# Optimization experiments

Measured on AMD Instinct MI355X. Metric: run time of the kernel, lower is better.

## Reference

```python
import jax, jax.numpy as jnp
import numpy as np

B, T, N, F_IN, C = 4, 40, 5000, 90, 256
E = 160000


def setup_inputs() -> dict:
    key = jax.random.key(0)
    ks = jax.random.split(key, 16)
    def p(k, shape, s=0.05):
        return jax.random.normal(k, shape, dtype=jnp.float32) * s
    z = lambda n: jnp.zeros((n,), jnp.float32)
    return {
        "x": jax.random.normal(ks[0], (B, T, N, F_IN), dtype=jnp.float32),
        "edge_index": jax.random.randint(ks[1], (1, 2, E), 0, N),
        "follower_ids": jax.random.randint(ks[2], (B,), 0, N),
        "attention": p(ks[3], (T,), 1.0),
        "Wz": p(ks[4], (F_IN, C)), "bz": z(C),
        "Wr": p(ks[5], (F_IN, C)), "br": z(C),
        "Wh": p(ks[6], (F_IN, C)), "bh": z(C),
        "Lz_w": p(ks[7], (2 * C, C)), "Lz_b": z(C),
        "Lr_w": p(ks[8], (2 * C, C)), "Lr_b": z(C),
        "Lh_w": p(ks[9], (2 * C, C)), "Lh_b": z(C),
        "M1_w": p(ks[10], (C, 64)), "M1_b": z(64),
        "M2_w": p(ks[11], (64, 32)), "M2_b": z(32),
        "M3_w": p(ks[12], (32, 5)), "M3_b": z(5),
    }


def _gcn_norm(edge_index, num_nodes):
    # GCNConv default: add self loops (weight 1), symmetric D^-1/2 (A+I) D^-1/2
    row, col = edge_index[0], edge_index[1]
    loop = jnp.arange(num_nodes)
    row = jnp.concatenate([row, loop])
    col = jnp.concatenate([col, loop])
    w = jnp.ones(row.shape[0], jnp.float32)
    deg = jnp.zeros(num_nodes, jnp.float32).at[col].add(w)
    dis = jnp.where(deg > 0, deg ** -0.5, 0.0)
    norm = dis[row] * w * dis[col]
    return row, col, norm


def _gcn(x, W, b, row, col, norm):
    # x: [B, N, F]; linear first, then normalized scatter-add aggregation
    xw = x @ W                                  # [B, N, C]
    msg = xw[:, row, :] * norm[None, :, None]   # [B, E+N, C]
    out = jnp.zeros_like(xw).at[:, col, :].add(msg)
    return out + b


def reference(x, edge_index, follower_ids, attention,
              Wz, bz, Wr, br, Wh, bh,
              Lz_w, Lz_b, Lr_w, Lr_b, Lh_w, Lh_b,
              M1_w, M1_b, M2_w, M2_b, M3_w, M3_b):
    ei = edge_index[0]
    row, col, norm = _gcn_norm(ei, N)

    def cell(H, xt):
        Z = jax.nn.sigmoid(jnp.concatenate([_gcn(xt, Wz, bz, row, col, norm), H], -1) @ Lz_w + Lz_b)
        R = jax.nn.sigmoid(jnp.concatenate([_gcn(xt, Wr, br, row, col, norm), H], -1) @ Lr_w + Lr_b)
        Ht = jnp.tanh(jnp.concatenate([_gcn(xt, Wh, bh, row, col, norm), H * R], -1) @ Lh_w + Lh_b)
        return Z * H + (1.0 - Z) * Ht

    probs = jax.nn.softmax(attention)

    def step(carry, inp):
        H, Hacc = carry
        xt, pt = inp
        H = cell(H, xt)
        return (H, Hacc + pt * H), None

    H0 = jnp.zeros((B, N, C), x.dtype)
    (_, Hacc), _ = jax.lax.scan(step, (H0, H0), (jnp.swapaxes(x, 0, 1), probs))

    h = Hacc[jnp.arange(B), follower_ids, :]          # [B, C]
    h = jax.nn.leaky_relu(h @ M1_w + M1_b)
    h = jax.nn.leaky_relu(h @ M2_w + M2_b)
    h = h @ M3_w + M3_b
    return 4.0 * jax.nn.sigmoid(h) + 1.0
```

## Files before the change

### kernel.cpp

```cpp
#include <hip/hip_runtime.h>
#include <hip/hip_bf16.h>
#include <cmath>

#define B_ 4
#define T_ 40
#define N_ 5000
#define F_ 90
#define C_ 256
#define E_ 160000
#define M_TOT (B_*N_)
#define M_PAD 20032
#define KP_ 96
#define NKT 11
#define NCT 48

typedef __attribute__((ext_vector_type(8))) short s16x8;
typedef __attribute__((ext_vector_type(4))) float f32x4;

__global__ void init_kernel(int* __restrict__ cnt, float* __restrict__ H, float* __restrict__ Hacc,
                            unsigned* __restrict__ HbU, unsigned* __restrict__ AxpU, unsigned* __restrict__ HRbU){
    const int i = blockIdx.x*blockDim.x + threadIdx.x;
    const int stride = gridDim.x*blockDim.x;
    for (int j = i; j < N_; j += stride) cnt[j] = 0;
    for (int j = i; j < M_PAD*C_; j += stride) H[j] = 0.f;
    for (int j = i; j < M_TOT*C_; j += stride) Hacc[j] = 0.f;
    for (int j = i; j < M_PAD*C_/2; j += stride) HbU[j] = 0u;
    const int padAxp = (M_PAD - M_TOT)*KP_/2;
    for (int j = i; j < padAxp; j += stride) AxpU[M_TOT*KP_/2 + j] = 0u;
    const int padHRb = (M_PAD - M_TOT)*C_/2;
    for (int j = i; j < padHRb; j += stride) HRbU[M_TOT*C_/2 + j] = 0u;
}

__global__ void count_kernel(const int* __restrict__ ei, int* __restrict__ cnt){
    int e = blockIdx.x*blockDim.x + threadIdx.x;
    if (e < E_) atomicAdd(&cnt[ei[E_ + e]], 1);
}

__global__ void dis_kernel(const int* __restrict__ cnt, float* __restrict__ dis, float* __restrict__ selfw){
    int n = blockIdx.x*blockDim.x + threadIdx.x;
    if (n < N_){
        float d = (float)cnt[n] + 1.0f;
        float r = 1.0f / sqrtf(d);
        dis[n] = r;
        selfw[n] = r*r;
    }
}

__global__ __launch_bounds__(256) void scan_kernel(const int* __restrict__ cnt, int* __restrict__ rowptr, int* __restrict__ pos){
    const int tid = threadIdx.x;
    const int base = tid*20;
    int v[20]; int s = 0;
    #pragma unroll
    for (int j = 0; j < 20; ++j){
        int idx = base + j;
        int c = (idx < N_) ? cnt[idx] : 0;
        v[j] = s; s += c;
    }
    __shared__ int sh[256];
    sh[tid] = s; __syncthreads();
    for (int off = 1; off < 256; off <<= 1){
        int x = (tid >= off) ? sh[tid-off] : 0;
        __syncthreads();
        sh[tid] += x;
        __syncthreads();
    }
    int excl = sh[tid] - s;
    #pragma unroll
    for (int j = 0; j < 20; ++j){
        int idx = base + j;
        if (idx < N_){ int val = excl + v[j]; rowptr[idx] = val; pos[idx] = val; }
    }
    if (tid == 255) rowptr[N_] = sh[255];
}

__global__ void scatter_kernel(const int* __restrict__ ei, const float* __restrict__ dis,
                               int* __restrict__ pos, int* __restrict__ csr_src, float* __restrict__ csr_w){
    int e = blockIdx.x*blockDim.x + threadIdx.x;
    if (e < E_){
        int r = ei[e];
        int c = ei[E_ + e];
        int p = atomicAdd(&pos[c], 1);
        csr_src[p] = r;
        csr_w[p]   = dis[r]*dis[c];
    }
}

__global__ void softmax_kernel(const float* __restrict__ att, float* __restrict__ probs){
    int t = threadIdx.x;
    float v = (t < T_) ? att[t] : -3.4e38f;
    float m = v;
    for (int o = 32; o > 0; o >>= 1) m = fmaxf(m, __shfl_xor(m, o));
    float e = (t < T_) ? expf(v - m) : 0.f;
    float s = e;
    for (int o = 32; o > 0; o >>= 1) s += __shfl_xor(s, o);
    if (t < T_) probs[t] = e / s;
}

__global__ __launch_bounds__(256) void foldw_kernel(const float* __restrict__ Wz, const float* __restrict__ Wr, const float* __restrict__ Wh,
                             const float* __restrict__ Lz, const float* __restrict__ Lr, const float* __restrict__ Lh,
                             float* __restrict__ Wp){
    int g = blockIdx.x / F_;
    int f = blockIdx.x % F_;
    int c = threadIdx.x;
    const float* W = (g == 0) ? Wz : (g == 1) ? Wr : Wh;
    const float* L = (g == 0) ? Lz : (g == 1) ? Lr : Lh;
    float acc = 0.f;
    for (int k = 0; k < C_; ++k) acc += W[f*C_ + k] * L[k*C_ + c];
    Wp[f*768 + g*256 + c] = acc;
}

__global__ __launch_bounds__(256) void foldb_kernel(const float* __restrict__ bz, const float* __restrict__ br, const float* __restrict__ bh,
                             const float* __restrict__ Lz, const float* __restrict__ Lr, const float* __restrict__ Lh,
                             const float* __restrict__ Lzb, const float* __restrict__ Lrb, const float* __restrict__ Lhb,
                             float* __restrict__ bp){
    int g = blockIdx.x;
    int c = threadIdx.x;
    const float* b = (g == 0) ? bz : (g == 1) ? br : bh;
    const float* L = (g == 0) ? Lz : (g == 1) ? Lr : Lh;
    const float* lb = (g == 0) ? Lzb : (g == 1) ? Lrb : Lhb;
    float acc = lb[c];
    for (int k = 0; k < C_; ++k) acc += b[k] * L[k*C_ + c];
    bp[g*256 + c] = acc;
}

__global__ __launch_bounds__(256) void pack_kernel(const float* __restrict__ Wp,
                             const float* __restrict__ Lz, const float* __restrict__ Lr, const float* __restrict__ Lh,
                             __hip_bfloat16* __restrict__ Bp){
    const int kt = blockIdx.x / NCT;
    const int ct = blockIdx.x % NCT;
    const int tid = threadIdx.x;
    const int l = tid & 63;
    const int jp = tid >> 6;
    const int c = ct*16 + (l & 15);
    #pragma unroll
    for (int jj = 0; jj < 2; ++jj){
        const int j = jp*2 + jj;
        const int k = kt*32 + (l >> 4)*8 + j;
        float v;
        if (k < F_) v = Wp[k*768 + c];
        else if (k < KP_) v = 0.f;
        else {
            int kk = k - KP_;
            int g = c >> 8, c2 = c & 255;
            const float* L = (g == 0) ? Lz : (g == 1) ? Lr : Lh;
            v = L[(256 + kk)*C_ + c2];
        }
        Bp[((size_t)(kt*NCT + ct)*64 + l)*8 + j] = __float2bfloat16(v);
    }
}

__global__ __launch_bounds__(256) void spmm_kernel(const float* __restrict__ X, const int* __restrict__ rowptr,
                            const int* __restrict__ csr_src, const float* __restrict__ csr_w,
                            const float* __restrict__ selfw, __hip_bfloat16* __restrict__ Axp, int t){
    const int n = blockIdx.x;
    const int tid = threadIdx.x;
    __shared__ int   s_src[256];
    __shared__ float s_w[256];
    const int beg = rowptr[n], end = rowptr[n+1];
    const int i0 = tid, i1 = tid + 256;
    const int b0 = i0 / F_, f0 = i0 - b0*F_;
    const int b1 = i1 / F_, f1 = i1 - b1*F_;
    const bool has1 = (i1 < B_*F_);
    const float sw = selfw[n];
    float acc0 = sw * X[((b0*T_ + t)*N_ + n)*F_ + f0];
    float acc1 = has1 ? sw * X[((b1*T_ + t)*N_ + n)*F_ + f1] : 0.f;
    for (int base = beg; base < end; base += 256){
        int cc = min(256, end - base);
        __syncthreads();
        if (tid < cc){ s_src[tid] = csr_src[base + tid]; s_w[tid] = csr_w[base + tid]; }
        __syncthreads();
        for (int j = 0; j < cc; ++j){
            int src = s_src[j]; float w = s_w[j];
            acc0 += w * X[((b0*T_ + t)*N_ + src)*F_ + f0];
            if (has1) acc1 += w * X[((b1*T_ + t)*N_ + src)*F_ + f1];
        }
    }
    Axp[(size_t)(b0*N_ + n)*KP_ + f0] = __float2bfloat16(acc0);
    if (has1) Axp[(size_t)(b1*N_ + n)*KP_ + f1] = __float2bfloat16(acc1);
    if (tid < B_*(KP_ - F_)){
        int b = tid / (KP_ - F_), f = F_ + tid % (KP_ - F_);
        Axp[(size_t)(b*N_ + n)*KP_ + f] = __float2bfloat16(0.f);
    }
}

template<int PHASE>
__global__ __launch_bounds__(256) void gemm_mfma(
    const s16x8* __restrict__ Axp,
    const s16x8* __restrict__ Hm,
    const s16x8* __restrict__ Bp,
    const float* __restrict__ bp,
    float* __restrict__ H,
    float* __restrict__ Zb,
    __hip_bfloat16* __restrict__ HRb,
    __hip_bfloat16* __restrict__ Hb,
    float* __restrict__ Hacc,
    const float* __restrict__ probs, int t)
{
    const int tid = threadIdx.x;
    const int l = tid & 63, w = tid >> 6;
    const int wr = w >> 1, wc = w & 1;
    const int row0 = blockIdx.x*64 + wr*32;
    const int colbase = (PHASE == 0 ? 0 : 512) + blockIdx.y*128 + wc*64;
    const int lr = l & 15, lk = l >> 4;
    const int ct0 = colbase >> 4;

    f32x4 acc[2][4] = {};

    const int ar0 = row0 + lr;
    const int ar1 = row0 + 16 + lr;

    #pragma unroll
    for (int kt = 0; kt < 3; ++kt){
        s16x8 a0 = Axp[(size_t)ar0*12 + kt*4 + lk];
        s16x8 a1 = Axp[(size_t)ar1*12 + kt*4 + lk];
        s16x8 b0 = Bp[((size_t)(kt*NCT + ct0 + 0) << 6) + l];
        s16x8 b1 = Bp[((size_t)(kt*NCT + ct0 + 1) << 6) + l];
        s16x8 b2 = Bp[((size_t)(kt*NCT + ct0 + 2) << 6) + l];
        s16x8 b3 = Bp[((size_t)(kt*NCT + ct0 + 3) << 6) + l];
        acc[0][0] = __builtin_amdgcn_mfma_f32_16x16x32_bf16(a0, b0, acc[0][0], 0, 0, 0);
        acc[0][1] = __builtin_amdgcn_mfma_f32_16x16x32_bf16(a0, b1, acc[0][1], 0, 0, 0);
        acc[0][2] = __builtin_amdgcn_mfma_f32_16x16x32_bf16(a0, b2, acc[0][2], 0, 0, 0);
        acc[0][3] = __builtin_amdgcn_mfma_f32_16x16x32_bf16(a0, b3, acc[0][3], 0, 0, 0);
        acc[1][0] = __builtin_amdgcn_mfma_f32_16x16x32_bf16(a1, b0, acc[1][0], 0, 0, 0);
        acc[1][1] = __builtin_amdgcn_mfma_f32_16x16x32_bf16(a1, b1, acc[1][1], 0, 0, 0);
        acc[1][2] = __builtin_amdgcn_mfma_f32_16x16x32_bf16(a1, b2, acc[1][2], 0, 0, 0);
        acc[1][3] = __builtin_amdgcn_mfma_f32_16x16x32_bf16(a1, b3, acc[1][3], 0, 0, 0);
    }
    #pragma unroll
    for (int kt = 0; kt < 8; ++kt){
        s16x8 a0 = Hm[(size_t)ar0*32 + kt*4 + lk];
        s16x8 a1 = Hm[(size_t)ar1*32 + kt*4 + lk];
        s16x8 b0 = Bp[((size_t)((kt+3)*NCT + ct0 + 0) << 6) + l];
        s16x8 b1 = Bp[((size_t)((kt+3)*NCT + ct0 + 1) << 6) + l];
        s16x8 b2 = Bp[((size_t)((kt+3)*NCT + ct0 + 2) << 6) + l];
        s16x8 b3 = Bp[((size_t)((kt+3)*NCT + ct0 + 3) << 6) + l];
        acc[0][0] = __builtin_amdgcn_mfma_f32_16x16x32_bf16(a0, b0, acc[0][0], 0, 0, 0);
        acc[0][1] = __builtin_amdgcn_mfma_f32_16x16x32_bf16(a0, b1, acc[0][1], 0, 0, 0);
        acc[0][2] = __builtin_amdgcn_mfma_f32_16x16x32_bf16(a0, b2, acc[0][2], 0, 0, 0);
        acc[0][3] = __builtin_amdgcn_mfma_f32_16x16x32_bf16(a0, b3, acc[0][3], 0, 0, 0);
        acc[1][0] = __builtin_amdgcn_mfma_f32_16x16x32_bf16(a1, b0, acc[1][0], 0, 0, 0);
        acc[1][1] = __builtin_amdgcn_mfma_f32_16x16x32_bf16(a1, b1, acc[1][1], 0, 0, 0);
        acc[1][2] = __builtin_amdgcn_mfma_f32_16x16x32_bf16(a1, b2, acc[1][2], 0, 0, 0);
        acc[1][3] = __builtin_amdgcn_mfma_f32_16x16x32_bf16(a1, b3, acc[1][3], 0, 0, 0);
    }

    const float pt = (PHASE == 1) ? probs[t] : 0.f;
    #pragma unroll
    for (int af = 0; af < 2; ++af){
        #pragma unroll
        for (int bf = 0; bf < 4; ++bf){
            const int c_full = colbase + bf*16 + lr;
            const float bias = bp[c_full];
            #pragma unroll
            for (int r = 0; r < 4; ++r){
                const int m = row0 + af*16 + lk*4 + r;
                if (m >= M_TOT) continue;
                float v = acc[af][bf][r] + bias;
                if (PHASE == 0){
                    float s = 1.f/(1.f + __expf(-v));
                    if (c_full < 256){
                        Zb[(size_t)m*C_ + c_full] = s;
                    } else {
                        int c2 = c_full - 256;
                        float hr = H[(size_t)m*C_ + c2] * s;
                        HRb[(size_t)m*C_ + c2] = __float2bfloat16(hr);
                    }
                } else {
                    int c2 = c_full - 512;
                    float ht = 1.f - 2.f/(__expf(2.f*v) + 1.f);
                    float z = Zb[(size_t)m*C_ + c2];
                    float h = H[(size_t)m*C_ + c2];
                    float hn = z*h + (1.f - z)*ht;
                    H[(size_t)m*C_ + c2] = hn;
                    Hb[(size_t)m*C_ + c2] = __float2bfloat16(hn);
                    Hacc[(size_t)m*C_ + c2] += pt*hn;
                }
            }
        }
    }
}

__global__ __launch_bounds__(256) void mlp_kernel(const float* __restrict__ Hacc, const int* __restrict__ fids,
                           const float* __restrict__ M1, const float* __restrict__ M1b,
                           const float* __restrict__ M2, const float* __restrict__ M2b,
                           const float* __restrict__ M3, const float* __restrict__ M3b,
                           float* __restrict__ out){
    const int b = blockIdx.x;
    const int tid = threadIdx.x;
    __shared__ float sh[C_];
    __shared__ float s1[64];
    __shared__ float s2[32];
    const int f = fids[b];
    sh[tid] = Hacc[((size_t)(b*N_ + f))*C_ + tid];
    __syncthreads();
    if (tid < 64){
        float a = M1b[tid];
        for (int k = 0; k < C_; ++k) a += sh[k]*M1[k*64 + tid];
        s1[tid] = (a > 0.f) ? a : 0.01f*a;
    }
    __syncthreads();
    if (tid < 32){
        float a = M2b[tid];
        for (int k = 0; k < 64; ++k) a += s1[k]*M2[k*32 + tid];
        s2[tid] = (a > 0.f) ? a : 0.01f*a;
    }
    __syncthreads();
    if (tid < 5){
        float a = M3b[tid];
        for (int k = 0; k < 32; ++k) a += s2[k]*M3[k*5 + tid];
        out[b*5 + tid] = 4.f/(1.f + expf(-a)) + 1.f;
    }
}

extern "C" void kernel_launch(void* const* d_in, const int* in_sizes, int n_in,
                              void* d_out, int out_size, void* d_ws, size_t ws_size,
                              hipStream_t stream) {
    const float* x   = (const float*)d_in[0];
    const int*   ei  = (const int*)d_in[1];
    const int*   fid = (const int*)d_in[2];
    const float* att = (const float*)d_in[3];
    const float* Wz  = (const float*)d_in[4];  const float* bz  = (const float*)d_in[5];
    const float* Wr  = (const float*)d_in[6];  const float* br  = (const float*)d_in[7];
    const float* Wh  = (const float*)d_in[8];  const float* bh  = (const float*)d_in[9];
    const float* Lz  = (const float*)d_in[10]; const float* Lzb = (const float*)d_in[11];
    const float* Lr  = (const float*)d_in[12]; const float* Lrb = (const float*)d_in[13];
    const float* Lh  = (const float*)d_in[14]; const float* Lhb = (const float*)d_in[15];
    const float* M1  = (const float*)d_in[16]; const float* M1b = (const float*)d_in[17];
    const float* M2  = (const float*)d_in[18]; const float* M2b = (const float*)d_in[19];
    const float* M3  = (const float*)d_in[20]; const float* M3b = (const float*)d_in[21];
    float* out = (float*)d_out;

    char* w = (char*)d_ws;
    auto alloc = [&](size_t bytes)->void*{ void* p = (void*)w; w += ((bytes + 255)/256)*256; return p; };
    int*   cnt     = (int*)  alloc((size_t)N_*4);
    int*   rowptr  = (int*)  alloc((size_t)(N_+1)*4);
    int*   pos     = (int*)  alloc((size_t)N_*4);
    float* dis     = (float*)alloc((size_t)N_*4);
    float* selfw   = (float*)alloc((size_t)N_*4);
    int*   csr_src = (int*)  alloc((size_t)E_*4);
    float* csr_w   = (float*)alloc((size_t)E_*4);
    float* probs   = (float*)alloc((size_t)T_*4);
    float* Wp      = (float*)alloc((size_t)F_*768*4);
    float* bp      = (float*)alloc((size_t)768*4);
    __hip_bfloat16* Bp  = (__hip_bfloat16*)alloc((size_t)NKT*NCT*64*8*2);
    __hip_bfloat16* Axp = (__hip_bfloat16*)alloc((size_t)M_PAD*KP_*2);
    float*          H   = (float*)alloc((size_t)M_PAD*C_*4);
    __hip_bfloat16* Hb  = (__hip_bfloat16*)alloc((size_t)M_PAD*C_*2);
    __hip_bfloat16* HRb = (__hip_bfloat16*)alloc((size_t)M_PAD*C_*2);
    float*          Zb  = (float*)alloc((size_t)M_PAD*C_*4);
    float*          Hacc= (float*)alloc((size_t)M_TOT*C_*4);

    init_kernel<<<2048, 256, 0, stream>>>(cnt, H, Hacc, (unsigned*)Hb, (unsigned*)Axp, (unsigned*)HRb);
    count_kernel<<<(E_ + 255)/256, 256, 0, stream>>>(ei, cnt);
    dis_kernel<<<(N_ + 255)/256, 256, 0, stream>>>(cnt, dis, selfw);
    scan_kernel<<<1, 256, 0, stream>>>(cnt, rowptr, pos);
    scatter_kernel<<<(E_ + 255)/256, 256, 0, stream>>>(ei, dis, pos, csr_src, csr_w);
    softmax_kernel<<<1, 64, 0, stream>>>(att, probs);
    foldw_kernel<<<3*F_, 256, 0, stream>>>(Wz, Wr, Wh, Lz, Lr, Lh, Wp);
    foldb_kernel<<<3, 256, 0, stream>>>(bz, br, bh, Lz, Lr, Lh, Lzb, Lrb, Lhb, bp);
    pack_kernel<<<NKT*NCT, 256, 0, stream>>>(Wp, Lz, Lr, Lh, Bp);

    const dim3 grid0((M_TOT + 63)/64, 4);
    const dim3 grid1((M_TOT + 63)/64, 2);

    for (int t = 0; t < T_; ++t){
        spmm_kernel<<<N_, 256, 0, stream>>>(x, rowptr, csr_src, csr_w, selfw, Axp, t);
        gemm_mfma<0><<<grid0, 256, 0, stream>>>((const s16x8*)Axp, (const s16x8*)Hb, (const s16x8*)Bp,
                                                bp, H, Zb, HRb, nullptr, nullptr, probs, t);
        gemm_mfma<1><<<grid1, 256, 0, stream>>>((const s16x8*)Axp, (const s16x8*)HRb, (const s16x8*)Bp,
                                                bp, H, Zb, nullptr, Hb, Hacc, probs, t);
    }
    mlp_kernel<<<B_, 256, 0, stream>>>(Hacc, fid, M1, M1b, M2, M2b, M3, M3b, out);
}
```

Before: 4.710 ms.

## Fuse all GRU timesteps into one persistent kernel with on-chip hidden state

Precomputes the graph aggregation for all timesteps in a single batched SpMM launch, then runs one persistent kernel per 64-row tile that loops over all 40 timesteps. Hidden state, gates and the attention accumulator stay in registers, and the bf16 H and H*R operands live in swizzled LDS. This removes 120 kernel launches and the per-step global round trips for H, Z, HRb and Hacc. In exchange it stores all timesteps' aggregated inputs at once (a larger buffer), and with only 313 blocks of 512 threads the GPU may be underfilled.

```diff
diff --git a/kernel.cpp b/kernel.cpp
--- a/kernel.cpp
+++ b/kernel.cpp
@@ -13,22 +13,27 @@
 #define KP_ 96
 #define NKT 11
 #define NCT 48
+#define NBLK 313
 
 typedef __attribute__((ext_vector_type(8))) short s16x8;
 typedef __attribute__((ext_vector_type(4))) float f32x4;
 
-__global__ void init_kernel(int* __restrict__ cnt, float* __restrict__ H, float* __restrict__ Hacc,
-                            unsigned* __restrict__ HbU, unsigned* __restrict__ AxpU, unsigned* __restrict__ HRbU){
+__device__ inline unsigned short f2bf(float v){
+    union { __hip_bfloat16 b; unsigned short u; } cv;
+    cv.b = __float2bfloat16(v);
+    return cv.u;
+}
+
+__global__ void init_kernel(int* __restrict__ cnt, unsigned* __restrict__ AxpU){
     const int i = blockIdx.x*blockDim.x + threadIdx.x;
     const int stride = gridDim.x*blockDim.x;
     for (int j = i; j < N_; j += stride) cnt[j] = 0;
-    for (int j = i; j < M_PAD*C_; j += stride) H[j] = 0.f;
-    for (int j = i; j < M_TOT*C_; j += stride) Hacc[j] = 0.f;
-    for (int j = i; j < M_PAD*C_/2; j += stride) HbU[j] = 0u;
-    const int padAxp = (M_PAD - M_TOT)*KP_/2;
-    for (int j = i; j < padAxp; j += stride) AxpU[M_TOT*KP_/2 + j] = 0u;
-    const int padHRb = (M_PAD - M_TOT)*C_/2;
-    for (int j = i; j < padHRb; j += stride) HRbU[M_TOT*C_/2 + j] = 0u;
+    const int padw = (M_PAD - M_TOT)*KP_/2;
+    const int tot = T_*padw;
+    for (int j = i; j < tot; j += stride){
+        int t = j / padw, o = j - t*padw;
+        AxpU[(size_t)t*(M_PAD*KP_/2) + (M_TOT*KP_/2) + o] = 0u;
+    }
 }
 
 __global__ void count_kernel(const int* __restrict__ ei, int* __restrict__ cnt){
@@ -149,11 +154,13 @@
     }
 }
 
-__global__ __launch_bounds__(256) void spmm_kernel(const float* __restrict__ X, const int* __restrict__ rowptr,
+__global__ __launch_bounds__(256) void spmm_all_kernel(const float* __restrict__ X, const int* __restrict__ rowptr,
                             const int* __restrict__ csr_src, const float* __restrict__ csr_w,
-                            const float* __restrict__ selfw, __hip_bfloat16* __restrict__ Axp, int t){
+                            const float* __restrict__ selfw, __hip_bfloat16* __restrict__ AxpAll){
     const int n = blockIdx.x;
+    const int t = blockIdx.y;
     const int tid = threadIdx.x;
+    __hip_bfloat16* Axp = AxpAll + (size_t)t*M_PAD*KP_;
     __shared__ int   s_src[256];
     __shared__ float s_w[256];
     const int beg = rowptr[n], end = rowptr[n+1];
@@ -162,17 +169,17 @@
     const int b1 = i1 / F_, f1 = i1 - b1*F_;
     const bool has1 = (i1 < B_*F_);
     const float sw = selfw[n];
-    float acc0 = sw * X[((b0*T_ + t)*N_ + n)*F_ + f0];
-    float acc1 = has1 ? sw * X[((b1*T_ + t)*N_ + n)*F_ + f1] : 0.f;
+    float acc0 = sw * X[((size_t)(b0*T_ + t)*N_ + n)*F_ + f0];
+    float acc1 = has1 ? sw * X[((size_t)(b1*T_ + t)*N_ + n)*F_ + f1] : 0.f;
     for (int base = beg; base < end; base += 256){
         int cc = min(256, end - base);
         __syncthreads();
         if (tid < cc){ s_src[tid] = csr_src[base + tid]; s_w[tid] = csr_w[base + tid]; }
         __syncthreads();
         for (int j = 0; j < cc; ++j){
-            int src = s_src[j]; float w = s_w[j];
-            acc0 += w * X[((b0*T_ + t)*N_ + src)*F_ + f0];
-            if (has1) acc1 += w * X[((b1*T_ + t)*N_ + src)*F_ + f1];
+            int src = s_src[j]; float wv = s_w[j];
+            acc0 += wv * X[((size_t)(b0*T_ + t)*N_ + src)*F_ + f0];
+            if (has1) acc1 += wv * X[((size_t)(b1*T_ + t)*N_ + src)*F_ + f1];
         }
     }
     Axp[(size_t)(b0*N_ + n)*KP_ + f0] = __float2bfloat16(acc0);
@@ -183,98 +190,150 @@
     }
 }
 
-template<int PHASE>
-__global__ __launch_bounds__(256) void gemm_mfma(
+__global__ __launch_bounds__(512, 2) void gru_fused(
     const s16x8* __restrict__ Axp,
-    const s16x8* __restrict__ Hm,
     const s16x8* __restrict__ Bp,
     const float* __restrict__ bp,
-    float* __restrict__ H,
-    float* __restrict__ Zb,
-    __hip_bfloat16* __restrict__ HRb,
-    __hip_bfloat16* __restrict__ Hb,
-    float* __restrict__ Hacc,
-    const float* __restrict__ probs, int t)
+    const float* __restrict__ probs,
+    float* __restrict__ Hacc)
 {
+    __shared__ __align__(16) unsigned short HbL[64*256];
+    __shared__ __align__(16) unsigned short HRL[64*256];
     const int tid = threadIdx.x;
     const int l = tid & 63, w = tid >> 6;
-    const int wr = w >> 1, wc = w & 1;
-    const int row0 = blockIdx.x*64 + wr*32;
-    const int colbase = (PHASE == 0 ? 0 : 512) + blockIdx.y*128 + wc*64;
     const int lr = l & 15, lk = l >> 4;
-    const int ct0 = colbase >> 4;
-
-    f32x4 acc[2][4] = {};
-
-    const int ar0 = row0 + lr;
-    const int ar1 = row0 + 16 + lr;
-
-    #pragma unroll
-    for (int kt = 0; kt < 3; ++kt){
-        s16x8 a0 = Axp[(size_t)ar0*12 + kt*4 + lk];
-        s16x8 a1 = Axp[(size_t)ar1*12 + kt*4 + lk];
-        s16x8 b0 = Bp[((size_t)(kt*NCT + ct0 + 0) << 6) + l];
-        s16x8 b1 = Bp[((size_t)(kt*NCT + ct0 + 1) << 6) + l];
-        s16x8 b2 = Bp[((size_t)(kt*NCT + ct0 + 2) << 6) + l];
-        s16x8 b3 = Bp[((size_t)(kt*NCT + ct0 + 3) << 6) + l];
-        acc[0][0] = __builtin_amdgcn_mfma_f32_16x16x32_bf16(a0, b0, acc[0][0], 0, 0, 0);
-        acc[0][1] = __builtin_amdgcn_mfma_f32_16x16x32_bf16(a0, b1, acc[0][1], 0, 0, 0);
-        acc[0][2] = __builtin_amdgcn_mfma_f32_16x16x32_bf16(a0, b2, acc[0][2], 0, 0, 0);
-        acc[0][3] = __builtin_amdgcn_mfma_f32_16x16x32_bf16(a0, b3, acc[0][3], 0, 0, 0);
-        acc[1][0] = __builtin_amdgcn_mfma_f32_16x16x32_bf16(a1, b0, acc[1][0], 0, 0, 0);
-        acc[1][1] = __builtin_amdgcn_mfma_f32_16x16x32_bf16(a1, b1, acc[1][1], 0, 0, 0);
-        acc[1][2] = __builtin_amdgcn_mfma_f32_16x16x32_bf16(a1, b2, acc[1][2], 0, 0, 0);
-        acc[1][3] = __builtin_amdgcn_mfma_f32_16x16x32_bf16(a1, b3, acc[1][3], 0, 0, 0);
-    }
-    #pragma unroll
-    for (int kt = 0; kt < 8; ++kt){
-        s16x8 a0 = Hm[(size_t)ar0*32 + kt*4 + lk];
-        s16x8 a1 = Hm[(size_t)ar1*32 + kt*4 + lk];
-        s16x8 b0 = Bp[((size_t)((kt+3)*NCT + ct0 + 0) << 6) + l];
-        s16x8 b1 = Bp[((size_t)((kt+3)*NCT + ct0 + 1) << 6) + l];
-        s16x8 b2 = Bp[((size_t)((kt+3)*NCT + ct0 + 2) << 6) + l];
-        s16x8 b3 = Bp[((size_t)((kt+3)*NCT + ct0 + 3) << 6) + l];
-        acc[0][0] = __builtin_amdgcn_mfma_f32_16x16x32_bf16(a0, b0, acc[0][0], 0, 0, 0);
-        acc[0][1] = __builtin_amdgcn_mfma_f32_16x16x32_bf16(a0, b1, acc[0][1], 0, 0, 0);
-        acc[0][2] = __builtin_amdgcn_mfma_f32_16x16x32_bf16(a0, b2, acc[0][2], 0, 0, 0);
-        acc[0][3] = __builtin_amdgcn_mfma_f32_16x16x32_bf16(a0, b3, acc[0][3], 0, 0, 0);
-        acc[1][0] = __builtin_amdgcn_mfma_f32_16x16x32_bf16(a1, b0, acc[1][0], 0, 0, 0);
-        acc[1][1] = __builtin_amdgcn_mfma_f32_16x16x32_bf16(a1, b1, acc[1][1], 0, 0, 0);
-        acc[1][2] = __builtin_amdgcn_mfma_f32_16x16x32_bf16(a1, b2, acc[1][2], 0, 0, 0);
-        acc[1][3] = __builtin_amdgcn_mfma_f32_16x16x32_bf16(a1, b3, acc[1][3], 0, 0, 0);
-    }
-
-    const float pt = (PHASE == 1) ? probs[t] : 0.f;
-    #pragma unroll
-    for (int af = 0; af < 2; ++af){
-        #pragma unroll
-        for (int bf = 0; bf < 4; ++bf){
-            const int c_full = colbase + bf*16 + lr;
-            const float bias = bp[c_full];
+    const int row0 = blockIdx.x * 64;
+
+    {
+        unsigned* p = (unsigned*)HbL;
+        for (int i = tid; i < 64*128; i += 512) p[i] = 0u;
+    }
+
+    f32x4 zf[4][2], Hreg[4][2], Ha[4][2];
+    #pragma unroll
+    for (int a = 0; a < 4; ++a)
+        #pragma unroll
+        for (int c = 0; c < 2; ++c){ zf[a][c] = {}; Hreg[a][c] = {}; Ha[a][c] = {}; }
+
+    float bz_[2], br_[2], bh_[2];
+    #pragma unroll
+    for (int cf = 0; cf < 2; ++cf){
+        const int c = w*32 + cf*16 + lr;
+        bz_[cf] = bp[c]; br_[cf] = bp[256 + c]; bh_[cf] = bp[512 + c];
+    }
+
+    int ardb[4], asw[4];
+    #pragma unroll
+    for (int af = 0; af < 4; ++af){
+        const int m = af*16 + lr;
+        ardb[af] = m*512 + lk*16;
+        asw[af]  = (m & 7) << 4;
+    }
+
+    for (int t = 0; t < T_; ++t){
+        __syncthreads();
+        const s16x8* At = Axp + (size_t)t * (M_PAD * 12);
+
+        f32x4 az[4][2] = {}, ar[4][2] = {};
+        #pragma unroll
+        for (int kt = 0; kt < NKT; ++kt){
+            s16x8 a[4];
+            if (kt < 3){
+                #pragma unroll
+                for (int af = 0; af < 4; ++af)
+                    a[af] = At[(size_t)(row0 + af*16 + lr)*12 + kt*4 + lk];
+            } else {
+                const int kb = (kt - 3)*64;
+                #pragma unroll
+                for (int af = 0; af < 4; ++af)
+                    a[af] = *(const s16x8*)((const char*)HbL + ((ardb[af] + kb) ^ asw[af]));
+            }
+            const s16x8* Bk = Bp + ((size_t)(kt*NCT) << 6);
+            const s16x8 bz0 = Bk[((size_t)(2*w + 0) << 6) + l];
+            const s16x8 bz1 = Bk[((size_t)(2*w + 1) << 6) + l];
+            const s16x8 br0 = Bk[((size_t)(16 + 2*w) << 6) + l];
+            const s16x8 br1 = Bk[((size_t)(17 + 2*w) << 6) + l];
+            #pragma unroll
+            for (int af = 0; af < 4; ++af){
+                az[af][0] = __builtin_amdgcn_mfma_f32_16x16x32_bf16(a[af], bz0, az[af][0], 0, 0, 0);
+                az[af][1] = __builtin_amdgcn_mfma_f32_16x16x32_bf16(a[af], bz1, az[af][1], 0, 0, 0);
+                ar[af][0] = __builtin_amdgcn_mfma_f32_16x16x32_bf16(a[af], br0, ar[af][0], 0, 0, 0);
+                ar[af][1] = __builtin_amdgcn_mfma_f32_16x16x32_bf16(a[af], br1, ar[af][1], 0, 0, 0);
+            }
+        }
+        #pragma unroll
+        for (int af = 0; af < 4; ++af){
+            #pragma unroll
+            for (int cf = 0; cf < 2; ++cf){
+                const int c2 = w*32 + cf*16 + lr;
+                #pragma unroll
+                for (int r = 0; r < 4; ++r){
+                    const float zv = 1.f/(1.f + __expf(-(az[af][cf][r] + bz_[cf])));
+                    const float sv = 1.f/(1.f + __expf(-(ar[af][cf][r] + br_[cf])));
+                    zf[af][cf][r] = zv;
+                    const float hr = Hreg[af][cf][r] * sv;
+                    const int m2 = af*16 + lk*4 + r;
+                    const int wb = (m2*512 + c2*2) ^ ((m2 & 7) << 4);
+                    *(unsigned short*)((char*)HRL + wb) = f2bf(hr);
+                }
+            }
+        }
+        __syncthreads();
+
+        f32x4 ah[4][2] = {};
+        #pragma unroll
+        for (int kt = 0; kt < NKT; ++kt){
+            s16x8 a[4];
+            if (kt < 3){
+                #pragma unroll
+                for (int af = 0; af < 4; ++af)
+                    a[af] = At[(size_t)(row0 + af*16 + lr)*12 + kt*4 + lk];
+            } else {
+                const int kb = (kt - 3)*64;
+                #pragma unroll
+                for (int af = 0; af < 4; ++af)
+                    a[af] = *(const s16x8*)((const char*)HRL + ((ardb[af] + kb) ^ asw[af]));
+            }
+            const s16x8* Bk = Bp + ((size_t)(kt*NCT) << 6);
+            const s16x8 bh0 = Bk[((size_t)(32 + 2*w) << 6) + l];
+            const s16x8 bh1 = Bk[((size_t)(33 + 2*w) << 6) + l];
+            #pragma unroll
+            for (int af = 0; af < 4; ++af){
+                ah[af][0] = __builtin_amdgcn_mfma_f32_16x16x32_bf16(a[af], bh0, ah[af][0], 0, 0, 0);
+                ah[af][1] = __builtin_amdgcn_mfma_f32_16x16x32_bf16(a[af], bh1, ah[af][1], 0, 0, 0);
+            }
+        }
+        const float pt = probs[t];
+        #pragma unroll
+        for (int af = 0; af < 4; ++af){
+            #pragma unroll
+            for (int cf = 0; cf < 2; ++cf){
+                const int c2 = w*32 + cf*16 + lr;
+                #pragma unroll
+                for (int r = 0; r < 4; ++r){
+                    const float v = ah[af][cf][r] + bh_[cf];
+                    const float ht = 1.f - 2.f/(__expf(2.f*v) + 1.f);
+                    const float zv = zf[af][cf][r];
+                    const float hn = zv*Hreg[af][cf][r] + (1.f - zv)*ht;
+                    Hreg[af][cf][r] = hn;
+                    Ha[af][cf][r] += pt*hn;
+                    const int m2 = af*16 + lk*4 + r;
+                    const int wb = (m2*512 + c2*2) ^ ((m2 & 7) << 4);
+                    *(unsigned short*)((char*)HbL + wb) = f2bf(hn);
+                }
+            }
+        }
+    }
+
+    #pragma unroll
+    for (int af = 0; af < 4; ++af){
+        #pragma unroll
+        for (int cf = 0; cf < 2; ++cf){
             #pragma unroll
             for (int r = 0; r < 4; ++r){
                 const int m = row0 + af*16 + lk*4 + r;
-                if (m >= M_TOT) continue;
-                float v = acc[af][bf][r] + bias;
-                if (PHASE == 0){
-                    float s = 1.f/(1.f + __expf(-v));
-                    if (c_full < 256){
-                        Zb[(size_t)m*C_ + c_full] = s;
-                    } else {
-                        int c2 = c_full - 256;
-                        float hr = H[(size_t)m*C_ + c2] * s;
-                        HRb[(size_t)m*C_ + c2] = __float2bfloat16(hr);
-                    }
-                } else {
-                    int c2 = c_full - 512;
-                    float ht = 1.f - 2.f/(__expf(2.f*v) + 1.f);
-                    float z = Zb[(size_t)m*C_ + c2];
-                    float h = H[(size_t)m*C_ + c2];
-                    float hn = z*h + (1.f - z)*ht;
-                    H[(size_t)m*C_ + c2] = hn;
-                    Hb[(size_t)m*C_ + c2] = __float2bfloat16(hn);
-                    Hacc[(size_t)m*C_ + c2] += pt*hn;
-                }
+                if (m < M_TOT)
+                    Hacc[(size_t)m*C_ + w*32 + cf*16 + lr] = Ha[af][cf][r];
             }
         }
     }
@@ -342,15 +401,11 @@
     float* probs   = (float*)alloc((size_t)T_*4);
     float* Wp      = (float*)alloc((size_t)F_*768*4);
     float* bp      = (float*)alloc((size_t)768*4);
-    __hip_bfloat16* Bp  = (__hip_bfloat16*)alloc((size_t)NKT*NCT*64*8*2);
-    __hip_bfloat16* Axp = (__hip_bfloat16*)alloc((size_t)M_PAD*KP_*2);
-    float*          H   = (float*)alloc((size_t)M_PAD*C_*4);
-    __hip_bfloat16* Hb  = (__hip_bfloat16*)alloc((size_t)M_PAD*C_*2);
-    __hip_bfloat16* HRb = (__hip_bfloat16*)alloc((size_t)M_PAD*C_*2);
-    float*          Zb  = (float*)alloc((size_t)M_PAD*C_*4);
-    float*          Hacc= (float*)alloc((size_t)M_TOT*C_*4);
-
-    init_kernel<<<2048, 256, 0, stream>>>(cnt, H, Hacc, (unsigned*)Hb, (unsigned*)Axp, (unsigned*)HRb);
+    __hip_bfloat16* Bp     = (__hip_bfloat16*)alloc((size_t)NKT*NCT*64*8*2);
+    __hip_bfloat16* AxpAll = (__hip_bfloat16*)alloc((size_t)T_*M_PAD*KP_*2);
+    float*          Hacc   = (float*)alloc((size_t)M_TOT*C_*4);
+
+    init_kernel<<<256, 256, 0, stream>>>(cnt, (unsigned*)AxpAll);
     count_kernel<<<(E_ + 255)/256, 256, 0, stream>>>(ei, cnt);
     dis_kernel<<<(N_ + 255)/256, 256, 0, stream>>>(cnt, dis, selfw);
     scan_kernel<<<1, 256, 0, stream>>>(cnt, rowptr, pos);
@@ -360,15 +415,7 @@
     foldb_kernel<<<3, 256, 0, stream>>>(bz, br, bh, Lz, Lr, Lh, Lzb, Lrb, Lhb, bp);
     pack_kernel<<<NKT*NCT, 256, 0, stream>>>(Wp, Lz, Lr, Lh, Bp);
 
-    const dim3 grid0((M_TOT + 63)/64, 4);
-    const dim3 grid1((M_TOT + 63)/64, 2);
-
-    for (int t = 0; t < T_; ++t){
-        spmm_kernel<<<N_, 256, 0, stream>>>(x, rowptr, csr_src, csr_w, selfw, Axp, t);
-        gemm_mfma<0><<<grid0, 256, 0, stream>>>((const s16x8*)Axp, (const s16x8*)Hb, (const s16x8*)Bp,
-                                                bp, H, Zb, HRb, nullptr, nullptr, probs, t);
-        gemm_mfma<1><<<grid1, 256, 0, stream>>>((const s16x8*)Axp, (const s16x8*)HRb, (const s16x8*)Bp,
-                                                bp, H, Zb, nullptr, Hb, Hacc, probs, t);
-    }
+    spmm_all_kernel<<<dim3(N_, T_), 256, 0, stream>>>(x, rowptr, csr_src, csr_w, selfw, AxpAll);
+    gru_fused<<<NBLK, 512, 0, stream>>>((const s16x8*)AxpAll, (const s16x8*)Bp, bp, probs, Hacc);
     mlp_kernel<<<B_, 256, 0, stream>>>(Hacc, fid, M1, M1b, M2, M2b, M3, M3b, out);
 }
```

Result: faster. 3.812 ms (-19.1%).
